# Performance work log

Measured on AMD Instinct MI355X. Metric: run time of the kernel, lower is better.

The kernel has to match this reference:

```python
import jax, jax.numpy as jnp
import numpy as np

B, S, D = 16, 2048, 1024  # batch, max_len, inp_size == hidden_size


def setup_inputs() -> dict:
    key = jax.random.key(0)
    k1, k2, k3, k4, k5, k6 = jax.random.split(key, 6)
    stdv = 1.0 / np.sqrt(D)
    return {
        "encoder_outputs": jax.random.normal(k1, (B, S, D), dtype=jnp.float32),
        "hidden": jax.random.normal(k2, (B, D), dtype=jnp.float32),
        "lengths": jax.random.randint(k3, (B,), 1, S + 1, dtype=jnp.int32),
        "W": jax.random.normal(k4, (D, 2 * D), dtype=jnp.float32) * stdv,
        "b": jax.random.normal(k5, (D,), dtype=jnp.float32) * stdv,
        "v": jax.random.normal(k6, (D,), dtype=jnp.float32) * stdv,
    }


def reference(encoder_outputs, hidden, lengths, W, b, v):
    # Linear on cat([H, enc]) == H @ Wh^T + enc @ We^T + b (avoids materializing the concat)
    Wh, We = W[:, :D], W[:, D:]              # [D_out, D] each
    hid_proj = hidden @ Wh.T                  # [B, D]
    enc_proj = jnp.einsum('bsd,ed->bse', encoder_outputs, We)  # [B, S, D]
    energy = jnp.tanh(enc_proj + hid_proj[:, None, :] + b)     # [B, S, D]
    scores = jnp.einsum('bsd,d->bs', energy, v)                # [B, S]
    # mask positions >= length to -inf before softmax
    valid = jnp.arange(S)[None, :] < lengths[:, None]          # [B, S]
    scores = jnp.where(valid, scores, -jnp.inf)
    attn = jax.nn.softmax(scores, axis=-1)                     # [B, S]
    context = jnp.einsum('bs,bsd->bd', attn, encoder_outputs)  # [B, D]
    return context[:, None, :]                                 # [B, 1, D] to match torch bmm output
```

## Files before the change

### kernel.cpp

```cpp
#include <hip/hip_runtime.h>
#include <cstdint>

#define DEV static __device__ __forceinline__

typedef __attribute__((__ext_vector_type__(8))) __bf16 bf16x8;
typedef __attribute__((__ext_vector_type__(4))) float f32x4;

static constexpr int Bc = 16, Sc = 2048, Dc = 1024;

DEV unsigned short f2bf(float x) {
  unsigned int u = __float_as_uint(x);
  unsigned int r = (u + 0x7fffu + ((u >> 16) & 1u)) >> 16;
  return (unsigned short)r;
}
DEV unsigned int pack2(float a, float b) {
  return (unsigned int)f2bf(a) | ((unsigned int)f2bf(b) << 16);
}
DEV float tanh_fast(float x) {
  return 1.f - 2.f / (__expf(2.f * x) + 1.f);
}
DEV void gload16(const void* g, void* l) {
  __builtin_amdgcn_global_load_lds(
      (const __attribute__((address_space(1))) unsigned int*)g,
      (__attribute__((address_space(3))) unsigned int*)l, 16, 0, 0);
}

__global__ __launch_bounds__(256) void k_cvt_enc(const float* __restrict__ in,
                                                 unsigned short* __restrict__ out,
                                                 const int* __restrict__ lengths) {
  int team = threadIdx.x >> 7;
  int lane = threadIdx.x & 127;
  int r0 = blockIdx.x * 16;
  int b = r0 >> 11;
  int len = lengths[b];
  for (int rr = team; rr < 16; rr += 2) {
    int s = (r0 + rr) & 2047;
    if (s >= len) continue;
    const float* src = in + (size_t)(r0 + rr) * Dc + lane * 8;
    unsigned short* dst = out + (size_t)(r0 + rr) * Dc + lane * 8;
    float4 f0 = *(const float4*)src;
    float4 f1 = *(const float4*)(src + 4);
    uint4 o;
    o.x = pack2(f0.x, f0.y);
    o.y = pack2(f0.z, f0.w);
    o.z = pack2(f1.x, f1.y);
    o.w = pack2(f1.z, f1.w);
    *(uint4*)dst = o;
  }
}

__global__ __launch_bounds__(256) void k_cvt_We(const float* __restrict__ W,
                                                unsigned short* __restrict__ out) {
  int i = (blockIdx.x * 256 + threadIdx.x) * 8;
  int e = i >> 10, d = i & 1023;
  const float* p = W + (size_t)e * 2048 + 1024 + d;
  float4 f0 = *(const float4*)p;
  float4 f1 = *(const float4*)(p + 4);
  uint4 o;
  o.x = pack2(f0.x, f0.y);
  o.y = pack2(f0.z, f0.w);
  o.z = pack2(f1.x, f1.y);
  o.w = pack2(f1.z, f1.w);
  *(uint4*)(out + i) = o;
}

__global__ __launch_bounds__(256) void k_hidproj(const float* __restrict__ hidden,
                                                 const float* __restrict__ W,
                                                 const float* __restrict__ bias,
                                                 float* __restrict__ hp) {
  __shared__ float wrow[Dc];
  int e = blockIdx.x, t = threadIdx.x;
  for (int i = t; i < Dc; i += 256) wrow[i] = W[(size_t)e * 2048 + i];
  __syncthreads();
  int w = t >> 6, lane = t & 63;
  float bv = bias[e];
  for (int bi = w; bi < Bc; bi += 4) {
    float s = 0.f;
    const float* hrow = hidden + (size_t)bi * Dc;
    for (int d = lane; d < Dc; d += 64) s += hrow[d] * wrow[d];
    for (int m = 1; m < 64; m <<= 1) s += __shfl_xor(s, m);
    if (lane == 0) hp[(size_t)bi * Dc + e] = s + bv;
  }
}

__global__ __launch_bounds__(256) void k_worklist(const int* __restrict__ lengths,
                                                  int* __restrict__ wl) {
  int t = threadIdx.x;
  int sblk = t >> 4, b = t & 15;
  int active = (sblk * 128 < lengths[b]) ? 1 : 0;
  unsigned long long mask = __ballot(active);
  int lane = t & 63, wid = t >> 6;
  int prefix = __popcll(mask & ((1ull << lane) - 1ull));
  __shared__ int woff[4];
  if (lane == 0) woff[wid] = __popcll(mask);
  __syncthreads();
  int base = 0;
  for (int i = 0; i < wid; i++) base += woff[i];
  if (active) wl[1 + base + prefix] = (b << 8) | sblk;
  if (t == 0) wl[0] = woff[0] + woff[1] + woff[2] + woff[3];
}

__global__ __launch_bounds__(256) void k_scores(const unsigned short* __restrict__ Ae,
                                                const unsigned short* __restrict__ We,
                                                const float* __restrict__ hp,
                                                const float* __restrict__ v,
                                                const int* __restrict__ wl,
                                                float* __restrict__ pscores) {
  int g = blockIdx.x & 255;
  int et = blockIdx.x >> 8;
  if (g >= wl[0]) return;
  int pk = wl[1 + g];
  int b = pk >> 8, sblk = pk & 255;
  int s0 = sblk * 128;
  int m0 = b * Sc + s0;
  int e0 = et * 128;

  __shared__ unsigned short As[128 * 32];
  __shared__ unsigned short Bs[128 * 32];
  __shared__ float hp_s[128], v_s[128], sc_s[128];

  int t = threadIdx.x;
  int w = t >> 6, lane = t & 63;
  if (t < 128) {
    hp_s[t] = hp[(size_t)b * Dc + e0 + t];
    v_s[t] = v[e0 + t];
    sc_s[t] = 0.f;
  }

  f32x4 acc[4][4] = {};
  int wr = w >> 1, wc = w & 1;
  const unsigned short* Ab = Ae + (size_t)m0 * Dc;
  const unsigned short* Bb = We + (size_t)e0 * Dc;
  int trow = t >> 2, tcol = (t & 3) * 8;

  for (int k0 = 0; k0 < Dc; k0 += 32) {
    const unsigned short* ga = Ab + (size_t)trow * Dc + k0 + tcol;
    const unsigned short* gb = Bb + (size_t)trow * Dc + k0 + tcol;
    gload16(ga, As + w * 512);
    gload16(ga + 64 * Dc, As + 2048 + w * 512);
    gload16(gb, Bs + w * 512);
    gload16(gb + 64 * Dc, Bs + 2048 + w * 512);
    __syncthreads();
    int kc = (lane >> 4) * 8;
    int ar = (wr * 64 + (lane & 15)) * 32 + kc;
    int br = (wc * 64 + (lane & 15)) * 32 + kc;
    bf16x8 af[4], bfr[4];
    for (int m = 0; m < 4; m++)
      af[m] = __builtin_bit_cast(bf16x8, *(const uint4*)(As + ar + m * 512));
    for (int n = 0; n < 4; n++)
      bfr[n] = __builtin_bit_cast(bf16x8, *(const uint4*)(Bs + br + n * 512));
    for (int m = 0; m < 4; m++)
      for (int n = 0; n < 4; n++)
        acc[m][n] = __builtin_amdgcn_mfma_f32_16x16x32_bf16(af[m], bfr[n], acc[m][n], 0, 0, 0);
    __syncthreads();
  }

  for (int m = 0; m < 4; m++) {
    float rs0 = 0.f, rs1 = 0.f, rs2 = 0.f, rs3 = 0.f;
    for (int n = 0; n < 4; n++) {
      int ec = wc * 64 + n * 16 + (lane & 15);
      float hpv = hp_s[ec], vv = v_s[ec];
      f32x4 a = acc[m][n];
      rs0 += vv * tanh_fast(a[0] + hpv);
      rs1 += vv * tanh_fast(a[1] + hpv);
      rs2 += vv * tanh_fast(a[2] + hpv);
      rs3 += vv * tanh_fast(a[3] + hpv);
    }
    for (int mask = 1; mask < 16; mask <<= 1) {
      rs0 += __shfl_xor(rs0, mask);
      rs1 += __shfl_xor(rs1, mask);
      rs2 += __shfl_xor(rs2, mask);
      rs3 += __shfl_xor(rs3, mask);
    }
    if ((lane & 15) == 0) {
      int rbase = wr * 64 + m * 16 + (lane >> 4) * 4;
      atomicAdd(&sc_s[rbase + 0], rs0);
      atomicAdd(&sc_s[rbase + 1], rs1);
      atomicAdd(&sc_s[rbase + 2], rs2);
      atomicAdd(&sc_s[rbase + 3], rs3);
    }
  }
  __syncthreads();
  if (t < 128) pscores[((size_t)et * Bc + b) * Sc + s0 + t] = sc_s[t];
}

__global__ __launch_bounds__(256) void k_softmax(const float* __restrict__ pscores,
                                                 const int* __restrict__ lengths,
                                                 float* __restrict__ attn) {
  int b = blockIdx.x, t = threadIdx.x;
  int len = lengths[b];
  float vals[8];
  float mx = -INFINITY;
  for (int i = 0; i < 8; i++) {
    int s = t + i * 256;
    float sc = 0.f;
    for (int p = 0; p < 8; p++) sc += pscores[((size_t)p * Bc + b) * Sc + s];
    sc = (s < len) ? sc : -INFINITY;
    vals[i] = sc;
    mx = fmaxf(mx, sc);
  }
  for (int m = 1; m < 64; m <<= 1) mx = fmaxf(mx, __shfl_xor(mx, m));
  __shared__ float rmax[4], rsum[4];
  int w = t >> 6, lane = t & 63;
  if (lane == 0) rmax[w] = mx;
  __syncthreads();
  mx = fmaxf(fmaxf(rmax[0], rmax[1]), fmaxf(rmax[2], rmax[3]));
  float sm = 0.f;
  for (int i = 0; i < 8; i++) {
    vals[i] = __expf(vals[i] - mx);
    sm += vals[i];
  }
  for (int m = 1; m < 64; m <<= 1) sm += __shfl_xor(sm, m);
  if (lane == 0) rsum[w] = sm;
  __syncthreads();
  sm = rsum[0] + rsum[1] + rsum[2] + rsum[3];
  float inv = 1.f / sm;
  for (int i = 0; i < 8; i++) attn[(size_t)b * Sc + t + i * 256] = vals[i] * inv;
}

__global__ __launch_bounds__(256) void k_ctx(const unsigned short* __restrict__ ebf,
                                             const float* __restrict__ attn,
                                             const int* __restrict__ lengths,
                                             float* __restrict__ pctx) {
  int b = blockIdx.x >> 4, sp = blockIdx.x & 15;
  int t = threadIdx.x;
  int d0 = t * 4;
  int sbeg = sp * 128;
  float* outp = pctx + ((size_t)sp * Bc + b) * Dc + d0;
  int len = lengths[b];
  if (sbeg >= len) {
    *(float4*)outp = make_float4(0.f, 0.f, 0.f, 0.f);
    return;
  }
  __shared__ float at_s[128];
  if (t < 128) at_s[t] = attn[(size_t)b * Sc + sbeg + t];
  __syncthreads();
  float4 a = make_float4(0.f, 0.f, 0.f, 0.f);
  const unsigned short* ebase = ebf + ((size_t)b * Sc + sbeg) * Dc + d0;
  int ns = min(128, len - sbeg);
  for (int i = 0; i < ns; i++) {
    float wt = at_s[i];
    uint2 u = *(const uint2*)(ebase + (size_t)i * Dc);
    a.x += wt * __uint_as_float(u.x << 16);
    a.y += wt * __uint_as_float(u.x & 0xffff0000u);
    a.z += wt * __uint_as_float(u.y << 16);
    a.w += wt * __uint_as_float(u.y & 0xffff0000u);
  }
  *(float4*)outp = a;
}

__global__ __launch_bounds__(256) void k_reduce(const float* __restrict__ pctx,
                                               float* __restrict__ out) {
  int i = blockIdx.x * 256 + threadIdx.x;
  int b = i >> 10, d = i & 1023;
  float s = 0.f;
  for (int p = 0; p < 16; p++) s += pctx[((size_t)p * Bc + b) * Dc + d];
  out[i] = s;
}

extern "C" void kernel_launch(void* const* d_in, const int* in_sizes, int n_in,
                              void* d_out, int out_size, void* d_ws, size_t ws_size,
                              hipStream_t stream) {
  const float* enc = (const float*)d_in[0];
  const float* hidden = (const float*)d_in[1];
  const int* lengths = (const int*)d_in[2];
  const float* W = (const float*)d_in[3];
  const float* bias = (const float*)d_in[4];
  const float* v = (const float*)d_in[5];
  float* out = (float*)d_out;

  char* ws = (char*)d_ws;
  unsigned short* ebf = (unsigned short*)ws;
  unsigned short* webf = (unsigned short*)(ws + 67108864);
  float* hp = (float*)(ws + 69206016);
  float* pscores = (float*)(ws + 69271552);
  float* attn = (float*)(ws + 70320128);
  float* pctx = (float*)(ws + 70451200);
  int* wl = (int*)(ws + 70516736);

  hipLaunchKernelGGL(k_cvt_enc, dim3(2048), dim3(256), 0, stream, enc, ebf, lengths);
  hipLaunchKernelGGL(k_cvt_We, dim3(512), dim3(256), 0, stream, W, webf);
  hipLaunchKernelGGL(k_hidproj, dim3(1024), dim3(256), 0, stream, hidden, W, bias, hp);
  hipLaunchKernelGGL(k_worklist, dim3(1), dim3(256), 0, stream, lengths, wl);
  hipLaunchKernelGGL(k_scores, dim3(2048), dim3(256), 0, stream, ebf, webf, hp, v,
                     wl, pscores);
  hipLaunchKernelGGL(k_softmax, dim3(16), dim3(256), 0, stream, pscores, lengths, attn);
  hipLaunchKernelGGL(k_ctx, dim3(256), dim3(256), 0, stream, ebf, attn, lengths, pctx);
  hipLaunchKernelGGL(k_reduce, dim3(64), dim3(256), 0, stream, pctx, out);
}
```

Measured before the change: 114.3 us.

## Widen score GEMM tile to 128x256 and pack work items densely across blocks

The fused score kernel now computes a 128x256 output tile per block. Each wave covers all 128 rows and a 64-column slice, which halves how often encoder tiles are reloaded across output-column tiles and halves the number of partial-score slices that softmax has to sum. Work items are spread evenly over a 1024-block grid computed from the worklist count, so blocks no longer exit early on empty slots. The larger accumulator set (128 floats per thread) and bigger LDS footprint are capped with launch_bounds(256,2), which risks register pressure and lower occupancy.

Result: slower. 117.0 us (+2.3%).

```diff
diff --git a/kernel.cpp b/kernel.cpp
--- a/kernel.cpp
+++ b/kernel.cpp
@@ -100,65 +100,73 @@
   if (t == 0) wl[0] = woff[0] + woff[1] + woff[2] + woff[3];
 }
 
-__global__ __launch_bounds__(256) void k_scores(const unsigned short* __restrict__ Ae,
-                                                const unsigned short* __restrict__ We,
-                                                const float* __restrict__ hp,
-                                                const float* __restrict__ v,
-                                                const int* __restrict__ wl,
-                                                float* __restrict__ pscores) {
-  int g = blockIdx.x & 255;
-  int et = blockIdx.x >> 8;
-  if (g >= wl[0]) return;
+__global__ __launch_bounds__(256, 2) void k_scores(const unsigned short* __restrict__ Ae,
+                                                   const unsigned short* __restrict__ We,
+                                                   const float* __restrict__ hp,
+                                                   const float* __restrict__ v,
+                                                   const int* __restrict__ wl,
+                                                   float* __restrict__ pscores) {
+  int count = wl[0];
+  int items = count * 4;
+  int bx = blockIdx.x;
+  int j_lo = (bx * items) >> 10;
+  int j_hi = ((bx + 1) * items) >> 10;
+  if (j_lo >= j_hi) return;
+  int et = j_lo / count;
+  int g = j_lo - et * count;
   int pk = wl[1 + g];
   int b = pk >> 8, sblk = pk & 255;
   int s0 = sblk * 128;
   int m0 = b * Sc + s0;
-  int e0 = et * 128;
+  int e0 = et * 256;
 
   __shared__ unsigned short As[128 * 32];
-  __shared__ unsigned short Bs[128 * 32];
-  __shared__ float hp_s[128], v_s[128], sc_s[128];
+  __shared__ unsigned short Bs[256 * 32];
+  __shared__ float hp_s[256], v_s[256], sc_s[128];
 
   int t = threadIdx.x;
   int w = t >> 6, lane = t & 63;
-  if (t < 128) {
-    hp_s[t] = hp[(size_t)b * Dc + e0 + t];
-    v_s[t] = v[e0 + t];
-    sc_s[t] = 0.f;
-  }
-
-  f32x4 acc[4][4] = {};
-  int wr = w >> 1, wc = w & 1;
-  const unsigned short* Ab = Ae + (size_t)m0 * Dc;
-  const unsigned short* Bb = We + (size_t)e0 * Dc;
-  int trow = t >> 2, tcol = (t & 3) * 8;
-
+  hp_s[t] = hp[(size_t)b * Dc + e0 + t];
+  v_s[t] = v[e0 + t];
+  if (t < 128) sc_s[t] = 0.f;
+
+  f32x4 acc[8][4] = {};
+  const unsigned short* gaT = Ae + (size_t)(m0 + (t >> 2)) * Dc + (t & 3) * 8;
+  const unsigned short* gbT = We + (size_t)(e0 + (t >> 2)) * Dc + (t & 3) * 8;
+
+  int kc = (lane >> 4) * 8;
+  int ar = (lane & 15) * 32 + kc;
+  int br = (w * 64 + (lane & 15)) * 32 + kc;
+
+#pragma unroll 1
   for (int k0 = 0; k0 < Dc; k0 += 32) {
-    const unsigned short* ga = Ab + (size_t)trow * Dc + k0 + tcol;
-    const unsigned short* gb = Bb + (size_t)trow * Dc + k0 + tcol;
-    gload16(ga, As + w * 512);
-    gload16(ga + 64 * Dc, As + 2048 + w * 512);
-    gload16(gb, Bs + w * 512);
-    gload16(gb + 64 * Dc, Bs + 2048 + w * 512);
+    gload16(gaT + k0, As + w * 512);
+    gload16(gaT + k0 + 64 * Dc, As + 2048 + w * 512);
+#pragma unroll
+    for (int jj = 0; jj < 4; ++jj)
+      gload16(gbT + k0 + jj * 64 * Dc, Bs + jj * 2048 + w * 512);
     __syncthreads();
-    int kc = (lane >> 4) * 8;
-    int ar = (wr * 64 + (lane & 15)) * 32 + kc;
-    int br = (wc * 64 + (lane & 15)) * 32 + kc;
-    bf16x8 af[4], bfr[4];
-    for (int m = 0; m < 4; m++)
+    bf16x8 af[8], bfr[4];
+#pragma unroll
+    for (int m = 0; m < 8; m++)
       af[m] = __builtin_bit_cast(bf16x8, *(const uint4*)(As + ar + m * 512));
+#pragma unroll
     for (int n = 0; n < 4; n++)
       bfr[n] = __builtin_bit_cast(bf16x8, *(const uint4*)(Bs + br + n * 512));
-    for (int m = 0; m < 4; m++)
+#pragma unroll
+    for (int m = 0; m < 8; m++)
+#pragma unroll
       for (int n = 0; n < 4; n++)
         acc[m][n] = __builtin_amdgcn_mfma_f32_16x16x32_bf16(af[m], bfr[n], acc[m][n], 0, 0, 0);
     __syncthreads();
   }
 
-  for (int m = 0; m < 4; m++) {
+#pragma unroll
+  for (int m = 0; m < 8; m++) {
     float rs0 = 0.f, rs1 = 0.f, rs2 = 0.f, rs3 = 0.f;
+#pragma unroll
     for (int n = 0; n < 4; n++) {
-      int ec = wc * 64 + n * 16 + (lane & 15);
+      int ec = w * 64 + n * 16 + (lane & 15);
       float hpv = hp_s[ec], vv = v_s[ec];
       f32x4 a = acc[m][n];
       rs0 += vv * tanh_fast(a[0] + hpv);
@@ -173,7 +181,7 @@
       rs3 += __shfl_xor(rs3, mask);
     }
     if ((lane & 15) == 0) {
-      int rbase = wr * 64 + m * 16 + (lane >> 4) * 4;
+      int rbase = m * 16 + (lane >> 4) * 4;
       atomicAdd(&sc_s[rbase + 0], rs0);
       atomicAdd(&sc_s[rbase + 1], rs1);
       atomicAdd(&sc_s[rbase + 2], rs2);
@@ -194,7 +202,7 @@
   for (int i = 0; i < 8; i++) {
     int s = t + i * 256;
     float sc = 0.f;
-    for (int p = 0; p < 8; p++) sc += pscores[((size_t)p * Bc + b) * Sc + s];
+    for (int p = 0; p < 4; p++) sc += pscores[((size_t)p * Bc + b) * Sc + s];
     sc = (s < len) ? sc : -INFINITY;
     vals[i] = sc;
     mx = fmaxf(mx, sc);
@@ -282,7 +290,7 @@
   hipLaunchKernelGGL(k_cvt_We, dim3(512), dim3(256), 0, stream, W, webf);
   hipLaunchKernelGGL(k_hidproj, dim3(1024), dim3(256), 0, stream, hidden, W, bias, hp);
   hipLaunchKernelGGL(k_worklist, dim3(1), dim3(256), 0, stream, lengths, wl);
-  hipLaunchKernelGGL(k_scores, dim3(2048), dim3(256), 0, stream, ebf, webf, hp, v,
+  hipLaunchKernelGGL(k_scores, dim3(1024), dim3(256), 0, stream, ebf, webf, hp, v,
                      wl, pscores);
   hipLaunchKernelGGL(k_softmax, dim3(16), dim3(256), 0, stream, pscores, lengths, attn);
   hipLaunchKernelGGL(k_ctx, dim3(256), dim3(256), 0, stream, ebf, attn, lengths, pctx);
```

## Double-buffer LDS tiles in score GEMM to overlap global loads with MFMA

Applied to the files above, without the earlier changes.

Switches the k_scores GEMM main loop to ping-pong LDS buffers, prefetching the next K-tile via global_load_lds while MFMAs run on the current one. Explicit vmcnt waits and s_barrier with sched_barrier replace the two __syncthreads per iteration, so each wave waits only on the older batch of loads. The goal is to hide global-memory latency behind compute, at the cost of doubling LDS use, which may lower occupancy, and of relying on hand-counted vmcnt values.

Measured after the change: 111.3 us. 2.6% less time.

```diff
diff --git a/kernel.cpp b/kernel.cpp
--- a/kernel.cpp
+++ b/kernel.cpp
@@ -115,8 +115,10 @@
   int m0 = b * Sc + s0;
   int e0 = et * 128;
 
-  __shared__ unsigned short As[128 * 32];
-  __shared__ unsigned short Bs[128 * 32];
+  __shared__ unsigned short As0[128 * 32];
+  __shared__ unsigned short As1[128 * 32];
+  __shared__ unsigned short Bs0[128 * 32];
+  __shared__ unsigned short Bs1[128 * 32];
   __shared__ float hp_s[128], v_s[128], sc_s[128];
 
   int t = threadIdx.x;
@@ -126,34 +128,72 @@
     v_s[t] = v[e0 + t];
     sc_s[t] = 0.f;
   }
+  asm volatile("s_waitcnt vmcnt(0)" ::: "memory");
 
   f32x4 acc[4][4] = {};
   int wr = w >> 1, wc = w & 1;
-  const unsigned short* Ab = Ae + (size_t)m0 * Dc;
-  const unsigned short* Bb = We + (size_t)e0 * Dc;
-  int trow = t >> 2, tcol = (t & 3) * 8;
-
-  for (int k0 = 0; k0 < Dc; k0 += 32) {
-    const unsigned short* ga = Ab + (size_t)trow * Dc + k0 + tcol;
-    const unsigned short* gb = Bb + (size_t)trow * Dc + k0 + tcol;
-    gload16(ga, As + w * 512);
-    gload16(ga + 64 * Dc, As + 2048 + w * 512);
-    gload16(gb, Bs + w * 512);
-    gload16(gb + 64 * Dc, Bs + 2048 + w * 512);
-    __syncthreads();
-    int kc = (lane >> 4) * 8;
-    int ar = (wr * 64 + (lane & 15)) * 32 + kc;
-    int br = (wc * 64 + (lane & 15)) * 32 + kc;
+  const unsigned short* ga0 = Ae + (size_t)(m0 + (t >> 2)) * Dc + (t & 3) * 8;
+  const unsigned short* gb0 = We + (size_t)(e0 + (t >> 2)) * Dc + (t & 3) * 8;
+
+  int kc = (lane >> 4) * 8;
+  int ar = (wr * 64 + (lane & 15)) * 32 + kc;
+  int br = (wc * 64 + (lane & 15)) * 32 + kc;
+
+  auto stage = [&](int k0, unsigned short* A, unsigned short* B) {
+    gload16(ga0 + k0, A + w * 512);
+    gload16(ga0 + k0 + 64 * Dc, A + 2048 + w * 512);
+    gload16(gb0 + k0, B + w * 512);
+    gload16(gb0 + k0 + 64 * Dc, B + 2048 + w * 512);
+  };
+  auto compute = [&](const unsigned short* A, const unsigned short* B) {
     bf16x8 af[4], bfr[4];
+#pragma unroll
     for (int m = 0; m < 4; m++)
-      af[m] = __builtin_bit_cast(bf16x8, *(const uint4*)(As + ar + m * 512));
+      af[m] = __builtin_bit_cast(bf16x8, *(const uint4*)(A + ar + m * 512));
+#pragma unroll
     for (int n = 0; n < 4; n++)
-      bfr[n] = __builtin_bit_cast(bf16x8, *(const uint4*)(Bs + br + n * 512));
+      bfr[n] = __builtin_bit_cast(bf16x8, *(const uint4*)(B + br + n * 512));
+#pragma unroll
     for (int m = 0; m < 4; m++)
+#pragma unroll
       for (int n = 0; n < 4; n++)
         acc[m][n] = __builtin_amdgcn_mfma_f32_16x16x32_bf16(af[m], bfr[n], acc[m][n], 0, 0, 0);
-    __syncthreads();
-  }
+  };
+
+  stage(0, As0, Bs0);
+
+#pragma unroll 1
+  for (int i2 = 0; i2 < 15; ++i2) {
+    stage((2 * i2 + 1) * 32, As1, Bs1);
+    asm volatile("s_waitcnt vmcnt(4)" ::: "memory");
+    __builtin_amdgcn_sched_barrier(0);
+    __builtin_amdgcn_s_barrier();
+    __builtin_amdgcn_sched_barrier(0);
+    compute(As0, Bs0);
+    __builtin_amdgcn_sched_barrier(0);
+    __builtin_amdgcn_s_barrier();
+    stage((2 * i2 + 2) * 32, As0, Bs0);
+    asm volatile("s_waitcnt vmcnt(4)" ::: "memory");
+    __builtin_amdgcn_sched_barrier(0);
+    __builtin_amdgcn_s_barrier();
+    __builtin_amdgcn_sched_barrier(0);
+    compute(As1, Bs1);
+    __builtin_amdgcn_sched_barrier(0);
+    __builtin_amdgcn_s_barrier();
+  }
+  stage(31 * 32, As1, Bs1);
+  asm volatile("s_waitcnt vmcnt(4)" ::: "memory");
+  __builtin_amdgcn_sched_barrier(0);
+  __builtin_amdgcn_s_barrier();
+  __builtin_amdgcn_sched_barrier(0);
+  compute(As0, Bs0);
+  __builtin_amdgcn_sched_barrier(0);
+  __builtin_amdgcn_s_barrier();
+  asm volatile("s_waitcnt vmcnt(0)" ::: "memory");
+  __builtin_amdgcn_sched_barrier(0);
+  __builtin_amdgcn_s_barrier();
+  __builtin_amdgcn_sched_barrier(0);
+  compute(As1, Bs1);
 
   for (int m = 0; m < 4; m++) {
     float rs0 = 0.f, rs1 = 0.f, rs2 = 0.f, rs3 = 0.f;
```
